# Optimization experiments

Measured on AMD Instinct MI355X. Metric: run time of the kernel, lower is better.

Reference implementation:

```python
import jax, jax.numpy as jnp
import numpy as np

N, E, C, R, B = 16384, 262144, 256, 9, 4


def _basis_mm(x, coeff, basis):
    # x: [E, Cin], coeff = att[edge_type]: [E, B], basis: [B, Cin, Cout]
    # equals x_e @ (sum_b coeff[e,b] * basis_b) = x_e @ W[edge_type[e]]
    h = jnp.einsum('ec,bco->ebo', x, basis)          # [E, B, Cout]
    return jnp.einsum('ebo,eb->eo', h, coeff)        # [E, Cout]


def _segment_softmax(score, gkey, nseg):
    smax = jax.ops.segment_max(score, gkey, num_segments=nseg)
    ex = jnp.exp(score - smax[gkey])
    den = jax.ops.segment_sum(ex, gkey, num_segments=nseg)
    return ex / den[gkey]


def _attn_branch(rel_emb, basis, att, aw, ab, etypes, seg):
    # relation-specific transform of edge features -> node messages
    m = _basis_mm(rel_emb, att[etypes], basis)                       # [E, Cn]
    # per-relation Linear (weight aw[r], bias ab[r]) + leaky_relu (slope 0.01)
    score = jax.nn.leaky_relu(jnp.sum(m * aw[etypes], -1) + ab[etypes])
    # original: softmax over dest index with -1e8 on edges of other relations,
    # then zeroed by mask == softmax within (dest node, relation) groups
    alpha = _segment_softmax(score, seg * R + etypes, N * R)         # [E]
    agg = jax.ops.segment_sum(alpha[:, None] * m, seg, num_segments=N)  # [N, Cn]
    onehot = jax.nn.one_hot(etypes, R, dtype=m.dtype)
    cnt = jax.ops.segment_sum(onehot, seg, num_segments=N)           # [N, R]
    div = (cnt > 0).astype(m.dtype).sum(-1)
    div = jnp.where(div == 0, jnp.ones_like(div), div)
    return agg / div[:, None]


def setup_inputs():
    key = jax.random.key(0)
    ks = jax.random.split(key, 16)
    p = lambda k, shp: jax.random.normal(k, shp, jnp.float32) * 0.05
    return {
        'edge_index': jax.random.randint(ks[0], (2, E), 0, N, dtype=jnp.int32),
        'nf': jax.random.normal(ks[1], (N, C), jnp.float32),
        'ef': jax.random.normal(ks[2], (E, C), jnp.float32),
        'edge_type_rel': jax.random.randint(ks[3], (E,), 0, R, dtype=jnp.int32),
        'edge_type_rel_inv': jax.random.randint(ks[4], (E,), 0, R, dtype=jnp.int32),
        'edge_norm': jax.random.uniform(ks[5], (E,), jnp.float32),
        'sub2rel_basis': p(ks[6], (B, C, C)),
        'sub2rel_att': p(ks[7], (R, B)),
        'obj2rel_basis': p(ks[8], (B, C, C)),
        'obj2rel_att': p(ks[9], (R, B)),
        'rel2sub_basis': p(ks[10], (B, C, C)),
        'rel2sub_att': p(ks[11], (R, B)),
        'rel2sub_attn_w': p(ks[12], (R, C)),
        'rel2sub_attn_b': jnp.zeros((R,), jnp.float32),
        'rel2obj_basis': p(ks[13], (B, C, C)),
        'rel2obj_att': p(ks[14], (R, B)),
        'rel2obj_attn_w': p(ks[15], (R, C)),
        'rel2obj_attn_b': jnp.zeros((R,), jnp.float32),
    }


def reference(edge_index, nf, ef, edge_type_rel, edge_type_rel_inv, edge_norm,
              sub2rel_basis, sub2rel_att, obj2rel_basis, obj2rel_att,
              rel2sub_basis, rel2sub_att, rel2sub_attn_w, rel2sub_attn_b,
              rel2obj_basis, rel2obj_att, rel2obj_attn_w, rel2obj_attn_b):
    src, dst = edge_index[0], edge_index[1]
    # sub2rel / obj2rel: per-edge relation-specific GEMM (mask+sum over rel in
    # the original collapses to a gather of W by edge type)
    s2r = _basis_mm(nf[src], sub2rel_att[edge_type_rel], sub2rel_basis)
    o2r = _basis_mm(nf[dst], obj2rel_att[edge_type_rel_inv], obj2rel_basis)
    rel_emb = ef + 0.5 * (s2r + o2r)
    # rel2sub aggregates at src (edgeindex_i = edge_index[0], rel types = inv)
    sub_agg = _attn_branch(rel_emb, rel2sub_basis, rel2sub_att,
                           rel2sub_attn_w, rel2sub_attn_b, edge_type_rel_inv, src)
    # rel2obj aggregates at dst (edgeindex_i = edge_index[1], rel types = fwd)
    obj_agg = _attn_branch(rel_emb, rel2obj_basis, rel2obj_att,
                           rel2obj_attn_w, rel2obj_attn_b, edge_type_rel, dst)
    node_emb = nf + 0.5 * (sub_agg + obj_agg)
    return node_emb, rel_emb
```

## Files before the change

kernel.cpp:

```cpp
#include <hip/hip_runtime.h>

#define N_ 16384
#define E_ 262144
#define C_ 256
#define R_ 9
#define B_ 4
#define NKEY (N_ * R_)
#define NKEY2 (2 * NKEY)

typedef unsigned short u16;
typedef unsigned int u32;

typedef __bf16 bf16x8 __attribute__((ext_vector_type(8)));
typedef float f32x4 __attribute__((ext_vector_type(4)));
typedef unsigned short u16x8 __attribute__((ext_vector_type(8)));

__device__ __forceinline__ u16 f2bf(float x) {
  u32 u = __float_as_uint(x);
  u32 r = (u + 0x7fffu + ((u >> 16) & 1u)) >> 16;
  return (u16)r;
}
__device__ __forceinline__ float bf2f(u16 h) {
  return __uint_as_float(((u32)h) << 16);
}

__device__ __forceinline__ void gld16(const void* g, void* l) {
  __builtin_amdgcn_global_load_lds(
      (const __attribute__((address_space(1))) void*)g,
      (__attribute__((address_space(3))) void*)l, 16, 0, 0);
}

__global__ __launch_bounds__(256) void prep_kernel(
    const float* __restrict__ b1, const float* __restrict__ a1,
    const float* __restrict__ b2, const float* __restrict__ a2,
    const float* __restrict__ b3, const float* __restrict__ a3,
    const float* __restrict__ aw3,
    const float* __restrict__ b4, const float* __restrict__ a4,
    const float* __restrict__ aw4,
    u16* __restrict__ W1, u16* __restrict__ W2,
    u16* __restrict__ W3, u16* __restrict__ W4,
    float* __restrict__ v3, float* __restrict__ v4) {
  int c = blockIdx.x, r = blockIdx.y, o = threadIdx.x;
  float s1 = 0.f, s2 = 0.f, s3 = 0.f, s4 = 0.f;
#pragma unroll
  for (int b = 0; b < B_; ++b) {
    long bi = ((long)b * C_ + c) * C_ + o;
    s1 += a1[r * B_ + b] * b1[bi];
    s2 += a2[r * B_ + b] * b2[bi];
    s3 += a3[r * B_ + b] * b3[bi];
    s4 += a4[r * B_ + b] * b4[bi];
  }
  W1[((long)r * C_ + o) * C_ + c] = f2bf(s1);
  W2[((long)r * C_ + o) * C_ + c] = f2bf(s2);
  W3[(long)o * (R_ * C_) + r * C_ + c] = f2bf(s3);
  W4[(long)o * (R_ * C_) + r * C_ + c] = f2bf(s4);

  __shared__ float red[256];
  red[o] = s3 * aw3[r * C_ + o];
  __syncthreads();
  for (int s = 128; s > 0; s >>= 1) {
    if (o < s) red[o] += red[o + s];
    __syncthreads();
  }
  float rv3 = red[0];
  __syncthreads();
  red[o] = s4 * aw4[r * C_ + o];
  __syncthreads();
  for (int s = 128; s > 0; s >>= 1) {
    if (o < s) red[o] += red[o + s];
    __syncthreads();
  }
  if (o == 0) {
    v3[r * C_ + c] = rv3;
    v4[r * C_ + c] = red[0];
  }
}

__global__ void cvt_bf16_kernel(const float* __restrict__ in, u16* __restrict__ out) {
  long i = ((long)blockIdx.x * 256 + threadIdx.x) * 4;
  float4 f = *(const float4*)(in + i);
  ushort4 h;
  h.x = f2bf(f.x); h.y = f2bf(f.y); h.z = f2bf(f.z); h.w = f2bf(f.w);
  *(ushort4*)(out + i) = h;
}

#define BM 128
#define BN 128
#define BK 32

__global__ __launch_bounds__(256) void gemmY_kernel(
    const u16* __restrict__ A, int lda,
    const u16* __restrict__ Bt0, const u16* __restrict__ Bt1, long bBatch, int K,
    u16* __restrict__ Out0, u16* __restrict__ Out1, long cBatch, int ldc) {
  __shared__ __attribute__((aligned(16))) u16 As[BM * BK];
  __shared__ __attribute__((aligned(16))) u16 Bs[BN * BK];

  const int t = threadIdx.x;
  const int m0 = blockIdx.x * BM;
  const int n0 = blockIdx.y * BN;
  const int zb = blockIdx.z;
  const long z = (zb < R_) ? zb : zb - R_;
  const u16* Bt = (zb < R_) ? Bt0 : Bt1;
  u16* Out = (zb < R_) ? Out0 : Out1;

  const int sr = t >> 2;
  const int sk = (t & 3) * 8;

  const int w = t >> 6, lane = t & 63;
  const int wm = (w >> 1) * 64, wn = (w & 1) * 64;
  const int lr = lane & 15;
  const int lk = (lane >> 4) * 8;

  f32x4 acc[4][4];
#pragma unroll
  for (int i = 0; i < 4; ++i)
#pragma unroll
    for (int j = 0; j < 4; ++j) acc[i][j] = (f32x4){0.f, 0.f, 0.f, 0.f};

  const u16* aR = A + (long)(m0 + sr) * lda + sk;
  const u16* bR = Bt + z * bBatch + (long)(n0 + sr) * K + sk;
  const long aStep = 64L * lda;
  const long bStep = 64L * K;

  u16* aD0 = &As[t * 8];
  u16* aD1 = &As[2048 + t * 8];
  u16* bD0 = &Bs[t * 8];
  u16* bD1 = &Bs[2048 + t * 8];

  for (int k0 = 0; k0 < K; k0 += BK) {
    gld16(aR, aD0);
    gld16(aR + aStep, aD1);
    gld16(bR, bD0);
    gld16(bR + bStep, bD1);
    aR += BK;
    bR += BK;
    __syncthreads();

    bf16x8 af[4], bg[4];
#pragma unroll
    for (int mi = 0; mi < 4; ++mi)
      af[mi] = *(const bf16x8*)&As[(wm + mi * 16 + lr) * BK + lk];
#pragma unroll
    for (int ni = 0; ni < 4; ++ni)
      bg[ni] = *(const bf16x8*)&Bs[(wn + ni * 16 + lr) * BK + lk];
#pragma unroll
    for (int mi = 0; mi < 4; ++mi)
#pragma unroll
      for (int ni = 0; ni < 4; ++ni)
        acc[mi][ni] = __builtin_amdgcn_mfma_f32_16x16x32_bf16(af[mi], bg[ni], acc[mi][ni], 0, 0, 0);

    __syncthreads();
  }

  long base = z * cBatch;
#pragma unroll
  for (int mi = 0; mi < 4; ++mi) {
    int rowb = m0 + wm + mi * 16 + ((lane >> 4) * 4);
#pragma unroll
    for (int ni = 0; ni < 4; ++ni) {
      int col = n0 + wn + ni * 16 + lr;
      f32x4 c = acc[mi][ni];
#pragma unroll
      for (int i = 0; i < 4; ++i) {
        long idx = base + (long)(rowb + i) * ldc + col;
        Out[idx] = f2bf(c[i]);
      }
    }
  }
}

template <int OMODE>
__global__ __launch_bounds__(256) void gemm64_kernel(
    const u16* __restrict__ A, int lda,
    const u16* __restrict__ Bt, int K,
    float* __restrict__ Out, int ldc,
    const float* __restrict__ nf, const float* __restrict__ dv) {
  __shared__ __attribute__((aligned(16))) u16 As[64 * BK];
  __shared__ __attribute__((aligned(16))) u16 Bs[BN * BK];

  const int t = threadIdx.x;
  const int m0 = blockIdx.x * 64;
  const int n0 = blockIdx.y * BN;

  const int sr = t >> 2;
  const int sk = (t & 3) * 8;

  const int w = t >> 6, lane = t & 63;
  const int wm = (w >> 1) * 32, wn = (w & 1) * 64;
  const int lr = lane & 15;
  const int lk = (lane >> 4) * 8;

  f32x4 acc[2][4];
#pragma unroll
  for (int i = 0; i < 2; ++i)
#pragma unroll
    for (int j = 0; j < 4; ++j) acc[i][j] = (f32x4){0.f, 0.f, 0.f, 0.f};

  const u16* aR = A + (long)(m0 + sr) * lda + sk;
  const u16* bR = Bt + (long)(n0 + sr) * K + sk;
  const long bStep = 64L * K;

  u16* aD = &As[t * 8];
  u16* bD0 = &Bs[t * 8];
  u16* bD1 = &Bs[2048 + t * 8];

  for (int k0 = 0; k0 < K; k0 += BK) {
    gld16(aR, aD);
    gld16(bR, bD0);
    gld16(bR + bStep, bD1);
    aR += BK;
    bR += BK;
    __syncthreads();

    bf16x8 af[2], bg[4];
#pragma unroll
    for (int mi = 0; mi < 2; ++mi)
      af[mi] = *(const bf16x8*)&As[(wm + mi * 16 + lr) * BK + lk];
#pragma unroll
    for (int ni = 0; ni < 4; ++ni)
      bg[ni] = *(const bf16x8*)&Bs[(wn + ni * 16 + lr) * BK + lk];
#pragma unroll
    for (int mi = 0; mi < 2; ++mi)
#pragma unroll
      for (int ni = 0; ni < 4; ++ni)
        acc[mi][ni] = __builtin_amdgcn_mfma_f32_16x16x32_bf16(af[mi], bg[ni], acc[mi][ni], 0, 0, 0);

    __syncthreads();
  }

#pragma unroll
  for (int mi = 0; mi < 2; ++mi) {
    int rowb = m0 + wm + mi * 16 + ((lane >> 4) * 4);
    float fs[4];
#pragma unroll
    for (int i = 0; i < 4; ++i) fs[i] = 0.5f * dv[rowb + i];
#pragma unroll
    for (int ni = 0; ni < 4; ++ni) {
      int col = n0 + wn + ni * 16 + lr;
      f32x4 c = acc[mi][ni];
#pragma unroll
      for (int i = 0; i < 4; ++i) {
        long idx = (long)(rowb + i) * ldc + col;
        if (OMODE == 3) Out[idx] = nf[idx] + fs[i] * c[i];
        else Out[idx] += fs[i] * c[i];
      }
    }
  }
}

__global__ __launch_bounds__(256) void relemb_kernel(
    const float* __restrict__ ef, const u16* __restrict__ Ysub,
    const u16* __restrict__ Yobj, const int* __restrict__ src,
    const int* __restrict__ dst, const int* __restrict__ et,
    const int* __restrict__ eti, const float* __restrict__ vS,
    const float* __restrict__ abS, const float* __restrict__ vO,
    const float* __restrict__ abO, float* __restrict__ rel,
    float* __restrict__ scoreS, float* __restrict__ scoreO,
    int* __restrict__ cnt) {
  int g = threadIdx.x >> 5;
  int h = threadIdx.x & 31;
  int c = h * 8;
  int e0 = blockIdx.x * 16 + g * 2;
  int e1 = e0 + 1;

  int sn0 = src[e0], dn0 = dst[e0], tf0 = et[e0], ti0 = eti[e0];
  int sn1 = src[e1], dn1 = dst[e1], tf1 = et[e1], ti1 = eti[e1];

  u16x8 ys0 = *(const u16x8*)(Ysub + ((long)tf0 * N_ + sn0) * C_ + c);
  u16x8 yo0 = *(const u16x8*)(Yobj + ((long)ti0 * N_ + dn0) * C_ + c);
  u16x8 ys1 = *(const u16x8*)(Ysub + ((long)tf1 * N_ + sn1) * C_ + c);
  u16x8 yo1 = *(const u16x8*)(Yobj + ((long)ti1 * N_ + dn1) * C_ + c);

  long ei0 = (long)e0 * C_ + c;
  long ei1 = (long)e1 * C_ + c;
  f32x4 f00 = __builtin_nontemporal_load((const f32x4*)(ef + ei0));
  f32x4 f01 = __builtin_nontemporal_load((const f32x4*)(ef + ei0 + 4));
  f32x4 f10 = __builtin_nontemporal_load((const f32x4*)(ef + ei1));
  f32x4 f11 = __builtin_nontemporal_load((const f32x4*)(ef + ei1 + 4));

  float a0 = f00[0] + 0.5f * (bf2f(ys0[0]) + bf2f(yo0[0]));
  float a1 = f00[1] + 0.5f * (bf2f(ys0[1]) + bf2f(yo0[1]));
  float a2 = f00[2] + 0.5f * (bf2f(ys0[2]) + bf2f(yo0[2]));
  float a3 = f00[3] + 0.5f * (bf2f(ys0[3]) + bf2f(yo0[3]));
  float a4 = f01[0] + 0.5f * (bf2f(ys0[4]) + bf2f(yo0[4]));
  float a5 = f01[1] + 0.5f * (bf2f(ys0[5]) + bf2f(yo0[5]));
  float a6 = f01[2] + 0.5f * (bf2f(ys0[6]) + bf2f(yo0[6]));
  float a7 = f01[3] + 0.5f * (bf2f(ys0[7]) + bf2f(yo0[7]));
  *(f32x4*)(rel + ei0) = (f32x4){a0, a1, a2, a3};
  *(f32x4*)(rel + ei0 + 4) = (f32x4){a4, a5, a6, a7};

  float b0 = f10[0] + 0.5f * (bf2f(ys1[0]) + bf2f(yo1[0]));
  float b1 = f10[1] + 0.5f * (bf2f(ys1[1]) + bf2f(yo1[1]));
  float b2 = f10[2] + 0.5f * (bf2f(ys1[2]) + bf2f(yo1[2]));
  float b3 = f10[3] + 0.5f * (bf2f(ys1[3]) + bf2f(yo1[3]));
  float b4 = f11[0] + 0.5f * (bf2f(ys1[4]) + bf2f(yo1[4]));
  float b5 = f11[1] + 0.5f * (bf2f(ys1[5]) + bf2f(yo1[5]));
  float b6 = f11[2] + 0.5f * (bf2f(ys1[6]) + bf2f(yo1[6]));
  float b7 = f11[3] + 0.5f * (bf2f(ys1[7]) + bf2f(yo1[7]));
  *(f32x4*)(rel + ei1) = (f32x4){b0, b1, b2, b3};
  *(f32x4*)(rel + ei1 + 4) = (f32x4){b4, b5, b6, b7};

  float4 w0, w1;
  w0 = *(const float4*)(vS + ti0 * C_ + c);
  w1 = *(const float4*)(vS + ti0 * C_ + c + 4);
  float pS0 = a0 * w0.x + a1 * w0.y + a2 * w0.z + a3 * w0.w +
              a4 * w1.x + a5 * w1.y + a6 * w1.z + a7 * w1.w;
  w0 = *(const float4*)(vO + tf0 * C_ + c);
  w1 = *(const float4*)(vO + tf0 * C_ + c + 4);
  float pO0 = a0 * w0.x + a1 * w0.y + a2 * w0.z + a3 * w0.w +
              a4 * w1.x + a5 * w1.y + a6 * w1.z + a7 * w1.w;
  w0 = *(const float4*)(vS + ti1 * C_ + c);
  w1 = *(const float4*)(vS + ti1 * C_ + c + 4);
  float pS1 = b0 * w0.x + b1 * w0.y + b2 * w0.z + b3 * w0.w +
              b4 * w1.x + b5 * w1.y + b6 * w1.z + b7 * w1.w;
  w0 = *(const float4*)(vO + tf1 * C_ + c);
  w1 = *(const float4*)(vO + tf1 * C_ + c + 4);
  float pO1 = b0 * w0.x + b1 * w0.y + b2 * w0.z + b3 * w0.w +
              b4 * w1.x + b5 * w1.y + b6 * w1.z + b7 * w1.w;

#pragma unroll
  for (int off = 16; off > 0; off >>= 1) {
    pS0 += __shfl_xor(pS0, off);
    pO0 += __shfl_xor(pO0, off);
    pS1 += __shfl_xor(pS1, off);
    pO1 += __shfl_xor(pO1, off);
  }
  if (h == 0) {
    float sS = pS0 + abS[ti0];
    sS = sS > 0.f ? sS : 0.01f * sS;
    scoreS[e0] = sS;
    atomicAdd(&cnt[sn0 * R_ + ti0], 1);
    float sO = pO0 + abO[tf0];
    sO = sO > 0.f ? sO : 0.01f * sO;
    scoreO[e0] = sO;
    atomicAdd(&cnt[NKEY + dn0 * R_ + tf0], 1);

    sS = pS1 + abS[ti1];
    sS = sS > 0.f ? sS : 0.01f * sS;
    scoreS[e1] = sS;
    atomicAdd(&cnt[sn1 * R_ + ti1], 1);
    sO = pO1 + abO[tf1];
    sO = sO > 0.f ? sO : 0.01f * sO;
    scoreO[e1] = sO;
    atomicAdd(&cnt[NKEY + dn1 * R_ + tf1], 1);
  }
}

__global__ __launch_bounds__(256) void div_kernel(const int* __restrict__ cnt,
                                                  float* __restrict__ divS,
                                                  float* __restrict__ divO) {
  int n = blockIdx.x * 256 + threadIdx.x;
  int ds = 0, dq = 0;
#pragma unroll
  for (int r = 0; r < R_; ++r) {
    ds += (cnt[n * R_ + r] > 0);
    dq += (cnt[NKEY + n * R_ + r] > 0);
  }
  divS[n] = ds ? 1.f / (float)ds : 1.f;
  divO[n] = dq ? 1.f / (float)dq : 1.f;
}

__global__ __launch_bounds__(256) void scan1_kernel(const int* __restrict__ cnt,
                                                    int* __restrict__ offs,
                                                    int* __restrict__ part) {
  __shared__ int lds[256];
  int b = blockIdx.x, t = threadIdx.x;
  int base = b * 1024 + t * 4;
  int4 v = *(const int4*)(cnt + base);
  int tsum = v.x + v.y + v.z + v.w;
  lds[t] = tsum;
  __syncthreads();
  for (int d = 1; d < 256; d <<= 1) {
    int x = (t >= d) ? lds[t - d] : 0;
    __syncthreads();
    lds[t] += x;
    __syncthreads();
  }
  int run = (t == 0) ? 0 : lds[t - 1];
  int4 o;
  o.x = run;
  o.y = run + v.x;
  o.z = o.y + v.y;
  o.w = o.z + v.z;
  *(int4*)(offs + base) = o;
  if (t == 255) part[b] = lds[255];
}

__global__ __launch_bounds__(512) void scan2_kernel(int* __restrict__ part) {
  __shared__ int lds[512];
  int t = threadIdx.x;
  lds[t] = (t < 288) ? part[t] : 0;
  __syncthreads();
  for (int d = 1; d < 512; d <<= 1) {
    int x = (t >= d) ? lds[t - d] : 0;
    __syncthreads();
    lds[t] += x;
    __syncthreads();
  }
  if (t < 288) part[t] = (t == 0) ? 0 : lds[t - 1];
}

__global__ __launch_bounds__(256) void scan3_kernel(const int* __restrict__ part,
                                                    int* __restrict__ offs,
                                                    int* __restrict__ cursor) {
  int i = blockIdx.x * 256 + threadIdx.x;
  int v = offs[i] + part[i >> 10];
  offs[i] = v;
  cursor[i] = v;
}

__global__ __launch_bounds__(256) void scatter_kernel(
    const int* __restrict__ et, const int* __restrict__ eti,
    const int* __restrict__ src, const int* __restrict__ dst,
    int* __restrict__ cursor, int* __restrict__ order) {
  int e = blockIdx.x * 256 + threadIdx.x;
  int kS = src[e] * R_ + eti[e];
  int kO = NKEY + dst[e] * R_ + et[e];
  order[atomicAdd(&cursor[kS], 1)] = e;
  order[atomicAdd(&cursor[kO], 1)] = e;
}

__global__ __launch_bounds__(256) void zgather_kernel(
    const float* __restrict__ rel, const float* __restrict__ scoreS,
    const float* __restrict__ scoreO, const int* __restrict__ order,
    const int* __restrict__ offs, const int* __restrict__ cnt,
    u16* __restrict__ zS, u16* __restrict__ zO) {
  int key = blockIdx.x * 4 + (threadIdx.x >> 6);
  int lane = threadIdx.x & 63;
  int c = lane * 4;
  int len = cnt[key];
  int start = offs[key];
  const float* score = scoreS;
  u16* z = zS;
  int k2 = key;
  if (key >= NKEY) { score = scoreO; z = zO; k2 = key - NKEY; }

  float ax = 0.f, ay = 0.f, az = 0.f, aw = 0.f;
  if (len == 1) {
    int e = order[start];
    float4 x = *(const float4*)(rel + (long)e * C_ + c);
    ax = x.x; ay = x.y; az = x.z; aw = x.w;
  } else if (len > 1 && len <= 64) {
    int e_l = 0;
    float s_l = 0.f;
    if (lane < len) {
      e_l = order[start + lane];
      s_l = __expf(score[e_l]);
    }
    float den = s_l;
#pragma unroll
    for (int off = 32; off > 0; off >>= 1) den += __shfl_xor(den, off);
    float inv = 1.f / den;
    int i = 0;
    for (; i + 2 <= len; i += 2) {
      int e0 = __shfl(e_l, i);
      int e1 = __shfl(e_l, i + 1);
      float a0 = __shfl(s_l, i) * inv;
      float a1 = __shfl(s_l, i + 1) * inv;
      float4 x0 = *(const float4*)(rel + (long)e0 * C_ + c);
      float4 x1 = *(const float4*)(rel + (long)e1 * C_ + c);
      ax += a0 * x0.x + a1 * x1.x;
      ay += a0 * x0.y + a1 * x1.y;
      az += a0 * x0.z + a1 * x1.z;
      aw += a0 * x0.w + a1 * x1.w;
    }
    if (i < len) {
      int e0 = __shfl(e_l, i);
      float a0 = __shfl(s_l, i) * inv;
      float4 x0 = *(const float4*)(rel + (long)e0 * C_ + c);
      ax += a0 * x0.x;
      ay += a0 * x0.y;
      az += a0 * x0.z;
      aw += a0 * x0.w;
    }
  } else if (len > 64) {
    float den = 0.f;
    for (int i = 0; i < len; ++i) {
      int e = order[start + i];
      float ex = __expf(score[e]);
      den += ex;
      float4 x = *(const float4*)(rel + (long)e * C_ + c);
      ax += ex * x.x; ay += ex * x.y; az += ex * x.z; aw += ex * x.w;
    }
    float inv = 1.f / den;
    ax *= inv; ay *= inv; az *= inv; aw *= inv;
  }
  int n = k2 / R_, r = k2 - n * R_;
  ushort4 h;
  h.x = f2bf(ax); h.y = f2bf(ay); h.z = f2bf(az); h.w = f2bf(aw);
  *(ushort4*)(z + (long)n * (R_ * C_) + r * C_ + c) = h;
}

extern "C" void kernel_launch(void* const* d_in, const int* in_sizes, int n_in,
                              void* d_out, int out_size, void* d_ws, size_t ws_size,
                              hipStream_t stream) {
  const int* edge_index = (const int*)d_in[0];
  const float* nf = (const float*)d_in[1];
  const float* ef = (const float*)d_in[2];
  const int* et = (const int*)d_in[3];
  const int* eti = (const int*)d_in[4];
  const float* s2r_basis = (const float*)d_in[6];
  const float* s2r_att = (const float*)d_in[7];
  const float* o2r_basis = (const float*)d_in[8];
  const float* o2r_att = (const float*)d_in[9];
  const float* r2s_basis = (const float*)d_in[10];
  const float* r2s_att = (const float*)d_in[11];
  const float* r2s_aw = (const float*)d_in[12];
  const float* r2s_ab = (const float*)d_in[13];
  const float* r2o_basis = (const float*)d_in[14];
  const float* r2o_att = (const float*)d_in[15];
  const float* r2o_aw = (const float*)d_in[16];
  const float* r2o_ab = (const float*)d_in[17];

  const int* src = edge_index;
  const int* dst = edge_index + E_;

  char* ws = (char*)d_ws;
  u16* WtSub = (u16*)(ws + 0);
  u16* WtObj = (u16*)(ws + 1179648);
  u16* WtR2S = (u16*)(ws + 2359296);
  u16* WtR2O = (u16*)(ws + 3538944);
  float* vS = (float*)(ws + 4718592);
  float* vO = (float*)(ws + 4727808);
  u16* nfb = (u16*)(ws + 4737024);
  float* scoreS = (float*)(ws + 13125632);
  float* scoreO = (float*)(ws + 14174208);
  int* cnt = (int*)(ws + 15222784);
  int* offs = (int*)(ws + 16402432);
  int* cursor = (int*)(ws + 17582080);
  int* order = (int*)(ws + 18761728);
  int* part = (int*)(ws + 20858880);
  float* divS = (float*)(ws + 20860928);
  float* divO = (float*)(ws + 20926464);
  u16* Ysub = (u16*)(ws + 20992000);
  u16* Yobj = (u16*)(ws + 96489472);
  u16* zS = Ysub;
  u16* zO = Yobj;

  float* node_out = (float*)d_out;
  float* rel_out = (float*)d_out + (long)N_ * C_;

  prep_kernel<<<dim3(C_, R_), 256, 0, stream>>>(
      s2r_basis, s2r_att, o2r_basis, o2r_att,
      r2s_basis, r2s_att, r2s_aw, r2o_basis, r2o_att, r2o_aw,
      WtSub, WtObj, WtR2S, WtR2O, vS, vO);
  cvt_bf16_kernel<<<(N_ * C_) / 1024, 256, 0, stream>>>(nf, nfb);
  (void)hipMemsetAsync(cnt, 0, (size_t)NKEY2 * 4, stream);

  gemmY_kernel<<<dim3(N_ / BM, C_ / BN, 2 * R_), 256, 0, stream>>>(
      nfb, C_, WtSub, WtObj, (long)C_ * C_, C_, Ysub, Yobj, (long)N_ * C_, C_);

  relemb_kernel<<<E_ / 16, 256, 0, stream>>>(ef, Ysub, Yobj, src, dst, et, eti,
                                             vS, r2s_ab, vO, r2o_ab, rel_out,
                                             scoreS, scoreO, cnt);
  div_kernel<<<N_ / 256, 256, 0, stream>>>(cnt, divS, divO);

  scan1_kernel<<<288, 256, 0, stream>>>(cnt, offs, part);
  scan2_kernel<<<1, 512, 0, stream>>>(part);
  scan3_kernel<<<NKEY2 / 256, 256, 0, stream>>>(part, offs, cursor);
  scatter_kernel<<<E_ / 256, 256, 0, stream>>>(et, eti, src, dst, cursor, order);
  zgather_kernel<<<NKEY2 / 4, 256, 0, stream>>>(rel_out, scoreS, scoreO, order,
                                                offs, cnt, zS, zO);

  gemm64_kernel<3><<<dim3(N_ / 64, C_ / BN), 256, 0, stream>>>(
      zS, R_ * C_, WtR2S, R_ * C_, node_out, C_, nf, divS);
  gemm64_kernel<4><<<dim3(N_ / 64, C_ / BN), 256, 0, stream>>>(
      zO, R_ * C_, WtR2O, R_ * C_, node_out, C_, nullptr, divO);

  (void)in_sizes; (void)n_in; (void)out_size; (void)ws_size;
}
```

Baseline: 933.6 us.

## Fuse two aggregation GEMMs, batch four keys per wave in zgather, drop nontemporal ef loads

The two per-branch aggregation GEMMs become one kernel that keeps two accumulator sets and writes node_out once as nf plus both scaled contributions. This removes a launch and the read-modify-write of node_out. zgather now has each wave handle four keys, issuing the cnt/offs/order/score loads for all four up front to expose more memory-level parallelism. The ef loads in relemb switch from nontemporal to ordinary loads. In exchange, the fused GEMM uses more registers and launches half as many blocks per output tile as the two kernels did before, which may lower parallelism.

```diff
diff --git a/kernel.cpp b/kernel.cpp
--- a/kernel.cpp
+++ b/kernel.cpp
@@ -169,12 +169,13 @@
   }
 }
 
-template <int OMODE>
-__global__ __launch_bounds__(256) void gemm64_kernel(
-    const u16* __restrict__ A, int lda,
-    const u16* __restrict__ Bt, int K,
-    float* __restrict__ Out, int ldc,
-    const float* __restrict__ nf, const float* __restrict__ dv) {
+__global__ __launch_bounds__(256) void gemmAgg_kernel(
+    const u16* __restrict__ AS, const u16* __restrict__ AO,
+    const u16* __restrict__ BtS, const u16* __restrict__ BtO,
+    float* __restrict__ Out,
+    const float* __restrict__ nf,
+    const float* __restrict__ divS, const float* __restrict__ divO) {
+  const int K = R_ * C_;
   __shared__ __attribute__((aligned(16))) u16 As[64 * BK];
   __shared__ __attribute__((aligned(16))) u16 Bs[BN * BK];
 
@@ -190,59 +191,89 @@
   const int lr = lane & 15;
   const int lk = (lane >> 4) * 8;
 
-  f32x4 acc[2][4];
-#pragma unroll
-  for (int i = 0; i < 2; ++i)
-#pragma unroll
-    for (int j = 0; j < 4; ++j) acc[i][j] = (f32x4){0.f, 0.f, 0.f, 0.f};
-
-  const u16* aR = A + (long)(m0 + sr) * lda + sk;
-  const u16* bR = Bt + (long)(n0 + sr) * K + sk;
-  const long bStep = 64L * K;
-
   u16* aD = &As[t * 8];
   u16* bD0 = &Bs[t * 8];
   u16* bD1 = &Bs[2048 + t * 8];
-
-  for (int k0 = 0; k0 < K; k0 += BK) {
-    gld16(aR, aD);
-    gld16(bR, bD0);
-    gld16(bR + bStep, bD1);
-    aR += BK;
-    bR += BK;
-    __syncthreads();
-
-    bf16x8 af[2], bg[4];
-#pragma unroll
-    for (int mi = 0; mi < 2; ++mi)
-      af[mi] = *(const bf16x8*)&As[(wm + mi * 16 + lr) * BK + lk];
-#pragma unroll
-    for (int ni = 0; ni < 4; ++ni)
-      bg[ni] = *(const bf16x8*)&Bs[(wn + ni * 16 + lr) * BK + lk];
-#pragma unroll
-    for (int mi = 0; mi < 2; ++mi)
+  const long bStep = 64L * K;
+
+  f32x4 accS[2][4], accO[2][4];
+#pragma unroll
+  for (int i = 0; i < 2; ++i)
+#pragma unroll
+    for (int j = 0; j < 4; ++j) {
+      accS[i][j] = (f32x4){0.f, 0.f, 0.f, 0.f};
+      accO[i][j] = (f32x4){0.f, 0.f, 0.f, 0.f};
+    }
+
+  {
+    const u16* aR = AS + (long)(m0 + sr) * K + sk;
+    const u16* bR = BtS + (long)(n0 + sr) * K + sk;
+    for (int k0 = 0; k0 < K; k0 += BK) {
+      gld16(aR, aD);
+      gld16(bR, bD0);
+      gld16(bR + bStep, bD1);
+      aR += BK;
+      bR += BK;
+      __syncthreads();
+      bf16x8 af[2], bg[4];
+#pragma unroll
+      for (int mi = 0; mi < 2; ++mi)
+        af[mi] = *(const bf16x8*)&As[(wm + mi * 16 + lr) * BK + lk];
 #pragma unroll
       for (int ni = 0; ni < 4; ++ni)
-        acc[mi][ni] = __builtin_amdgcn_mfma_f32_16x16x32_bf16(af[mi], bg[ni], acc[mi][ni], 0, 0, 0);
-
-    __syncthreads();
+        bg[ni] = *(const bf16x8*)&Bs[(wn + ni * 16 + lr) * BK + lk];
+#pragma unroll
+      for (int mi = 0; mi < 2; ++mi)
+#pragma unroll
+        for (int ni = 0; ni < 4; ++ni)
+          accS[mi][ni] = __builtin_amdgcn_mfma_f32_16x16x32_bf16(af[mi], bg[ni], accS[mi][ni], 0, 0, 0);
+      __syncthreads();
+    }
+  }
+  {
+    const u16* aR = AO + (long)(m0 + sr) * K + sk;
+    const u16* bR = BtO + (long)(n0 + sr) * K + sk;
+    for (int k0 = 0; k0 < K; k0 += BK) {
+      gld16(aR, aD);
+      gld16(bR, bD0);
+      gld16(bR + bStep, bD1);
+      aR += BK;
+      bR += BK;
+      __syncthreads();
+      bf16x8 af[2], bg[4];
+#pragma unroll
+      for (int mi = 0; mi < 2; ++mi)
+        af[mi] = *(const bf16x8*)&As[(wm + mi * 16 + lr) * BK + lk];
+#pragma unroll
+      for (int ni = 0; ni < 4; ++ni)
+        bg[ni] = *(const bf16x8*)&Bs[(wn + ni * 16 + lr) * BK + lk];
+#pragma unroll
+      for (int mi = 0; mi < 2; ++mi)
+#pragma unroll
+        for (int ni = 0; ni < 4; ++ni)
+          accO[mi][ni] = __builtin_amdgcn_mfma_f32_16x16x32_bf16(af[mi], bg[ni], accO[mi][ni], 0, 0, 0);
+      __syncthreads();
+    }
   }
 
 #pragma unroll
   for (int mi = 0; mi < 2; ++mi) {
     int rowb = m0 + wm + mi * 16 + ((lane >> 4) * 4);
-    float fs[4];
-#pragma unroll
-    for (int i = 0; i < 4; ++i) fs[i] = 0.5f * dv[rowb + i];
+    float fsS[4], fsO[4];
+#pragma unroll
+    for (int i = 0; i < 4; ++i) {
+      fsS[i] = 0.5f * divS[rowb + i];
+      fsO[i] = 0.5f * divO[rowb + i];
+    }
 #pragma unroll
     for (int ni = 0; ni < 4; ++ni) {
       int col = n0 + wn + ni * 16 + lr;
-      f32x4 c = acc[mi][ni];
+      f32x4 cS = accS[mi][ni];
+      f32x4 cO = accO[mi][ni];
 #pragma unroll
       for (int i = 0; i < 4; ++i) {
-        long idx = (long)(rowb + i) * ldc + col;
-        if (OMODE == 3) Out[idx] = nf[idx] + fs[i] * c[i];
-        else Out[idx] += fs[i] * c[i];
+        long idx = (long)(rowb + i) * C_ + col;
+        Out[idx] = nf[idx] + fsS[i] * cS[i] + fsO[i] * cO[i];
       }
     }
   }
@@ -273,10 +304,10 @@
 
   long ei0 = (long)e0 * C_ + c;
   long ei1 = (long)e1 * C_ + c;
-  f32x4 f00 = __builtin_nontemporal_load((const f32x4*)(ef + ei0));
-  f32x4 f01 = __builtin_nontemporal_load((const f32x4*)(ef + ei0 + 4));
-  f32x4 f10 = __builtin_nontemporal_load((const f32x4*)(ef + ei1));
-  f32x4 f11 = __builtin_nontemporal_load((const f32x4*)(ef + ei1 + 4));
+  f32x4 f00 = *(const f32x4*)(ef + ei0);
+  f32x4 f01 = *(const f32x4*)(ef + ei0 + 4);
+  f32x4 f10 = *(const f32x4*)(ef + ei1);
+  f32x4 f11 = *(const f32x4*)(ef + ei1 + 4);
 
   float a0 = f00[0] + 0.5f * (bf2f(ys0[0]) + bf2f(yo0[0]));
   float a1 = f00[1] + 0.5f * (bf2f(ys0[1]) + bf2f(yo0[1]));
@@ -420,43 +451,27 @@
   order[atomicAdd(&cursor[kO], 1)] = e;
 }
 
-__global__ __launch_bounds__(256) void zgather_kernel(
-    const float* __restrict__ rel, const float* __restrict__ scoreS,
-    const float* __restrict__ scoreO, const int* __restrict__ order,
-    const int* __restrict__ offs, const int* __restrict__ cnt,
-    u16* __restrict__ zS, u16* __restrict__ zO) {
-  int key = blockIdx.x * 4 + (threadIdx.x >> 6);
-  int lane = threadIdx.x & 63;
-  int c = lane * 4;
-  int len = cnt[key];
-  int start = offs[key];
-  const float* score = scoreS;
-  u16* z = zS;
-  int k2 = key;
-  if (key >= NKEY) { score = scoreO; z = zO; k2 = key - NKEY; }
-
+__device__ __forceinline__ void zkey_process(
+    const float* __restrict__ rel, const float* __restrict__ score,
+    const int* __restrict__ order, int len, int sta, int eL, float scL,
+    int lane, int c, u16* __restrict__ z, int k2) {
   float ax = 0.f, ay = 0.f, az = 0.f, aw = 0.f;
   if (len == 1) {
-    int e = order[start];
+    int e = __shfl(eL, 0);
     float4 x = *(const float4*)(rel + (long)e * C_ + c);
     ax = x.x; ay = x.y; az = x.z; aw = x.w;
   } else if (len > 1 && len <= 64) {
-    int e_l = 0;
-    float s_l = 0.f;
-    if (lane < len) {
-      e_l = order[start + lane];
-      s_l = __expf(score[e_l]);
-    }
-    float den = s_l;
+    float ex = (lane < len) ? __expf(scL) : 0.f;
+    float den = ex;
 #pragma unroll
     for (int off = 32; off > 0; off >>= 1) den += __shfl_xor(den, off);
     float inv = 1.f / den;
     int i = 0;
     for (; i + 2 <= len; i += 2) {
-      int e0 = __shfl(e_l, i);
-      int e1 = __shfl(e_l, i + 1);
-      float a0 = __shfl(s_l, i) * inv;
-      float a1 = __shfl(s_l, i + 1) * inv;
+      int e0 = __shfl(eL, i);
+      int e1 = __shfl(eL, i + 1);
+      float a0 = __shfl(ex, i) * inv;
+      float a1 = __shfl(ex, i + 1) * inv;
       float4 x0 = *(const float4*)(rel + (long)e0 * C_ + c);
       float4 x1 = *(const float4*)(rel + (long)e1 * C_ + c);
       ax += a0 * x0.x + a1 * x1.x;
@@ -465,8 +480,8 @@
       aw += a0 * x0.w + a1 * x1.w;
     }
     if (i < len) {
-      int e0 = __shfl(e_l, i);
-      float a0 = __shfl(s_l, i) * inv;
+      int e0 = __shfl(eL, i);
+      float a0 = __shfl(ex, i) * inv;
       float4 x0 = *(const float4*)(rel + (long)e0 * C_ + c);
       ax += a0 * x0.x;
       ay += a0 * x0.y;
@@ -476,19 +491,54 @@
   } else if (len > 64) {
     float den = 0.f;
     for (int i = 0; i < len; ++i) {
-      int e = order[start + i];
-      float ex = __expf(score[e]);
-      den += ex;
+      int e = order[sta + i];
+      float ex2 = __expf(score[e]);
+      den += ex2;
       float4 x = *(const float4*)(rel + (long)e * C_ + c);
-      ax += ex * x.x; ay += ex * x.y; az += ex * x.z; aw += ex * x.w;
+      ax += ex2 * x.x; ay += ex2 * x.y; az += ex2 * x.z; aw += ex2 * x.w;
     }
     float inv = 1.f / den;
     ax *= inv; ay *= inv; az *= inv; aw *= inv;
   }
   int n = k2 / R_, r = k2 - n * R_;
-  ushort4 h;
-  h.x = f2bf(ax); h.y = f2bf(ay); h.z = f2bf(az); h.w = f2bf(aw);
-  *(ushort4*)(z + (long)n * (R_ * C_) + r * C_ + c) = h;
+  ushort4 hv;
+  hv.x = f2bf(ax); hv.y = f2bf(ay); hv.z = f2bf(az); hv.w = f2bf(aw);
+  *(ushort4*)(z + (long)n * (R_ * C_) + r * C_ + c) = hv;
+}
+
+__global__ __launch_bounds__(256) void zgather_kernel(
+    const float* __restrict__ rel, const float* __restrict__ scoreS,
+    const float* __restrict__ scoreO, const int* __restrict__ order,
+    const int* __restrict__ offs, const int* __restrict__ cnt,
+    u16* __restrict__ zS, u16* __restrict__ zO) {
+  int wid = threadIdx.x >> 6;
+  int lane = threadIdx.x & 63;
+  int c = lane * 4;
+  int key0 = (blockIdx.x * 4 + wid) * 4;
+  const float* score = scoreS;
+  u16* z = zS;
+  int kb = key0;
+  if (key0 >= NKEY) { score = scoreO; z = zO; kb = key0 - NKEY; }
+
+  int len0 = cnt[key0], len1 = cnt[key0 + 1], len2 = cnt[key0 + 2], len3 = cnt[key0 + 3];
+  int sta0 = offs[key0], sta1 = offs[key0 + 1], sta2 = offs[key0 + 2], sta3 = offs[key0 + 3];
+
+  int e0 = 0, e1 = 0, e2 = 0, e3 = 0;
+  if (len0 <= 64 && lane < len0) e0 = order[sta0 + lane];
+  if (len1 <= 64 && lane < len1) e1 = order[sta1 + lane];
+  if (len2 <= 64 && lane < len2) e2 = order[sta2 + lane];
+  if (len3 <= 64 && lane < len3) e3 = order[sta3 + lane];
+
+  float s0 = 0.f, s1 = 0.f, s2 = 0.f, s3 = 0.f;
+  if (len0 > 1 && len0 <= 64 && lane < len0) s0 = score[e0];
+  if (len1 > 1 && len1 <= 64 && lane < len1) s1 = score[e1];
+  if (len2 > 1 && len2 <= 64 && lane < len2) s2 = score[e2];
+  if (len3 > 1 && len3 <= 64 && lane < len3) s3 = score[e3];
+
+  zkey_process(rel, score, order, len0, sta0, e0, s0, lane, c, z, kb + 0);
+  zkey_process(rel, score, order, len1, sta1, e1, s1, lane, c, z, kb + 1);
+  zkey_process(rel, score, order, len2, sta2, e2, s2, lane, c, z, kb + 2);
+  zkey_process(rel, score, order, len3, sta3, e3, s3, lane, c, z, kb + 3);
 }
 
 extern "C" void kernel_launch(void* const* d_in, const int* in_sizes, int n_in,
@@ -559,13 +609,11 @@
   scan2_kernel<<<1, 512, 0, stream>>>(part);
   scan3_kernel<<<NKEY2 / 256, 256, 0, stream>>>(part, offs, cursor);
   scatter_kernel<<<E_ / 256, 256, 0, stream>>>(et, eti, src, dst, cursor, order);
-  zgather_kernel<<<NKEY2 / 4, 256, 0, stream>>>(rel_out, scoreS, scoreO, order,
-                                                offs, cnt, zS, zO);
-
-  gemm64_kernel<3><<<dim3(N_ / 64, C_ / BN), 256, 0, stream>>>(
-      zS, R_ * C_, WtR2S, R_ * C_, node_out, C_, nf, divS);
-  gemm64_kernel<4><<<dim3(N_ / 64, C_ / BN), 256, 0, stream>>>(
-      zO, R_ * C_, WtR2O, R_ * C_, node_out, C_, nullptr, divO);
+  zgather_kernel<<<NKEY2 / 16, 256, 0, stream>>>(rel_out, scoreS, scoreO, order,
+                                                 offs, cnt, zS, zO);
+
+  gemmAgg_kernel<<<dim3(N_ / 64, C_ / BN), 256, 0, stream>>>(
+      zS, zO, WtR2S, WtR2O, node_out, nf, divS, divO);
 
   (void)in_sizes; (void)n_in; (void)out_size; (void)ws_size;
 }
```

Result: faster. 908.0 us (-2.7%).
